# Optimization experiments

Measured on AMD Instinct MI355X. Metric: run time of the kernel, lower is better.

## Reference

```python
import jax, jax.numpy as jnp
import numpy as np

RF = 3          # receptive_field_size (cubic)
STRIDE = 1
TEMP = 1.0      # softmax temperature ('soft' sampling, eval mode: no Gumbel noise)
TREE_DEPTH = 4

# Truth table of all 16 binary gates: GATES[g, t] = value of gate g on input
# pattern t = 2*a + b (a = first child, b = second child), t in {0,1,2,3}.
GATES = np.array([[(g >> t) & 1 for t in range(4)] for g in range(16)],
                 dtype=np.float32)  # (16, 4)


def _lut_eval(a, b, w):
    """Differentiable 2-input LUT. a, b: (B,K,P,nodes); w: (nodes,K,16)."""
    probs = jax.nn.softmax(w / TEMP, axis=-1)          # (nodes,K,16)
    lut = probs @ jnp.asarray(GATES)                   # (nodes,K,4) relaxed truth table
    lut = jnp.moveaxis(lut, 0, 1)[:, None]             # (K,1,nodes,4) -> bcast over B,P
    l0, l1, l2, l3 = lut[..., 0], lut[..., 1], lut[..., 2], lut[..., 3]
    na, nb = 1.0 - a, 1.0 - b
    # E[lut(a,b)] under independent Bernoulli inputs
    return l0 * na * nb + l1 * na * b + l2 * a * nb + l3 * a * b


def setup_inputs() -> dict:
    key = jax.random.key(0)
    ks = jax.random.split(key, 8)
    B, C, H, W, D = 4, 3, 32, 32, 32
    K, S = 32, 16  # num_kernels, lut_rank**tree_depth leaves
    x = jax.random.uniform(ks[0], (B, C, H, W, D), dtype=jnp.float32)
    # (lut_rank=2, K, S, 4) coords (h, w, d, c); rf=3 and channels=3 so all in [0,3)
    kernel_coords = jax.random.randint(ks[1], (2, K, S, 4), 0, 3, dtype=jnp.int32)
    w0 = jax.random.normal(ks[2], (16, K, 16), dtype=jnp.float32)
    w1 = jax.random.normal(ks[3], (8, K, 16), dtype=jnp.float32)
    w2 = jax.random.normal(ks[4], (4, K, 16), dtype=jnp.float32)
    w3 = jax.random.normal(ks[5], (2, K, 16), dtype=jnp.float32)
    w4 = jax.random.normal(ks[6], (1, K, 16), dtype=jnp.float32)
    return {"x": x, "kernel_coords": kernel_coords,
            "w0": w0, "w1": w1, "w2": w2, "w3": w3, "w4": w4}


def reference(x, kernel_coords, w0, w1, w2, w3, w4):
    B, C, H, W, D = x.shape
    OH, OW, OD = (H - RF) // STRIDE + 1, (W - RF) // STRIDE + 1, (D - RF) // STRIDE + 1
    kc = kernel_coords
    # linear offset of each leaf coord inside flattened (C,H,W,D) volume
    base = ((kc[..., 3] * H + kc[..., 0]) * W + kc[..., 1]) * D + kc[..., 2]  # (2,K,S)
    oh = jnp.arange(OH) * STRIDE
    ow = jnp.arange(OW) * STRIDE
    od = jnp.arange(OD) * STRIDE
    patch = ((oh[:, None, None] * W + ow[None, :, None]) * D
             + od[None, None, :]).reshape(-1)                                  # (P,)
    lin = base[:, :, None, :] + patch[None, None, :, None]                     # (2,K,P,S)
    g = x.reshape(B, -1)[:, lin]                                               # (B,2,K,P,S)
    out = _lut_eval(g[:, 0], g[:, 1], w0)                                      # (B,K,P,S)
    for w in (w1, w2, w3, w4):  # binary tree reduction over TREE_DEPTH levels
        out = _lut_eval(out[..., 0::2], out[..., 1::2], w)
    return out.reshape(B, out.shape[1], OH, OW, OD)
```

## Files before the change

### kernel.cpp

```cpp
#include <hip/hip_runtime.h>


#define B_  4
#define C_  3
#define H_  32
#define W_  32
#define D_  32
#define K_  32
#define S_  16
#define WS  33
#define TPB 512

typedef float v8f __attribute__((ext_vector_type(8), aligned(4)));

__device__ __forceinline__ v8f lut8(v8f a, v8f b, float l0, float d1, float d2, float d3) {
    const v8f t0 = a * d2 + l0;
    const v8f t1 = a * d3 + d1;
    return b * t1 + t0;
}

__global__ __launch_bounds__(TPB, 4) void logic_conv3d(
    const float* __restrict__ x,
    const int*   __restrict__ kc,
    const float* __restrict__ w0,
    const float* __restrict__ w1,
    const float* __restrict__ w2,
    const float* __restrict__ w3,
    const float* __restrict__ w4,
    float*       __restrict__ out)
{
    __shared__ float4 s_lut[31];
    __shared__ int    s_lb[16];
    __shared__ int    s_gb[16];
    __shared__ __align__(16) float slab[18 * 32 * WS];

    const int bk  = blockIdx.x;
    const int b   = bk >> 5;
    const int k   = bk & 31;
    const int tid = threadIdx.x;
    const int oh0 = blockIdx.y * 4;

    if (tid < 31) {
        const float* wp; int ln;
        if      (tid < 16) { wp = w0; ln = tid;      }
        else if (tid < 24) { wp = w1; ln = tid - 16; }
        else if (tid < 28) { wp = w2; ln = tid - 24; }
        else if (tid < 30) { wp = w3; ln = tid - 28; }
        else               { wp = w4; ln = 0;        }
        const float* wrow = wp + (ln * K_ + k) * 16;
        float lg[16];
        float m = -1e30f;
        #pragma unroll
        for (int g = 0; g < 16; ++g) { lg[g] = wrow[g]; m = fmaxf(m, lg[g]); }
        float z = 0.f;
        #pragma unroll
        for (int g = 0; g < 16; ++g) { lg[g] = __expf(lg[g] - m); z += lg[g]; }
        const float inv = 1.0f / z;
        float l0 = 0.f, l1 = 0.f, l2 = 0.f, l3 = 0.f;
        #pragma unroll
        for (int g = 0; g < 16; ++g) {
            float p = lg[g] * inv;
            if (g & 1) l0 += p;
            if (g & 2) l1 += p;
            if (g & 4) l2 += p;
            if (g & 8) l3 += p;
        }
        s_lut[tid] = make_float4(l0, l1 - l0, l2 - l0, (l3 - l2) - (l1 - l0));
    } else if (tid >= 32 && tid < 64) {
        const int idx  = tid - 32;
        const int tree = idx >> 4;
        const int s    = idx & 15;
        const int off  = ((tree * K_ + k) * S_ + s) * 4;
        const int h = kc[off + 0], w = kc[off + 1], d = kc[off + 2], c = kc[off + 3];
        if (tree == 0)
            s_lb[s] = ((c * 6 + h) * 32 + w) * WS + d;
        else
            s_gb[s] = ((c * H_ + h) * W_ + w) * D_ + d;
    }

    {
        const float* xb = x + (size_t)b * (C_ * H_ * W_ * D_);
        #pragma unroll
        for (int it = 0; it < 9; ++it) {
            const int idx   = it * TPB + tid;
            const int plane = idx >> 8;
            const int f4    = idx & 255;
            const int c     = plane / 6;
            const int dh    = plane - c * 6;
            const int h     = min(oh0 + dh, H_ - 1);
            const int w     = f4 >> 3;
            const int d4    = (f4 & 7) << 2;
            const float4 val = *(const float4*)(xb + ((c * H_ + h) * W_ + w) * D_ + d4);
            *(float4*)&slab[(plane * 32 + w) * WS + d4] = val;
        }
    }
    __syncthreads();

    int sA[16], sB[16];
    #pragma unroll
    for (int i = 0; i < 4; ++i) {
        const int4 qa = *(const int4*)&s_lb[i * 4];
        sA[i * 4 + 0] = __builtin_amdgcn_readfirstlane(qa.x);
        sA[i * 4 + 1] = __builtin_amdgcn_readfirstlane(qa.y);
        sA[i * 4 + 2] = __builtin_amdgcn_readfirstlane(qa.z);
        sA[i * 4 + 3] = __builtin_amdgcn_readfirstlane(qa.w);
        const int4 qb = *(const int4*)&s_gb[i * 4];
        sB[i * 4 + 0] = __builtin_amdgcn_readfirstlane(qb.x);
        sB[i * 4 + 1] = __builtin_amdgcn_readfirstlane(qb.y);
        sB[i * 4 + 2] = __builtin_amdgcn_readfirstlane(qb.z);
        sB[i * 4 + 3] = __builtin_amdgcn_readfirstlane(qb.w);
    }

    const int ohl = tid >> 7;
    const int r   = tid & 127;
    const int ow  = r >> 2;
    const int gq  = r & 3;
    const int od0 = (gq < 3) ? (gq << 3) : 22;
    const int oh  = oh0 + ohl;

    if (ow < 30 && oh < 30) {
        const int vo  = ohl * (32 * WS) + ow * WS + od0;
        const int gvo = ohl * (W_ * D_) + ow * D_ + od0;
        const float* xg = x + (size_t)b * (C_ * H_ * W_ * D_) + oh0 * (W_ * D_);

        v8f v1[8];
        #pragma unroll
        for (int j = 0; j < 8; ++j) {
            const int s0 = 2 * j, s1 = 2 * j + 1;
            const v8f A0 = *(const v8f*)&slab[sA[s0] + vo];
            const v8f B0 = *(const v8f*)(xg + sB[s0] + gvo);
            const float4 L0 = s_lut[s0];
            const v8f t0 = lut8(A0, B0, L0.x, L0.y, L0.z, L0.w);
            const v8f A1 = *(const v8f*)&slab[sA[s1] + vo];
            const v8f B1 = *(const v8f*)(xg + sB[s1] + gvo);
            const float4 L1 = s_lut[s1];
            const v8f t1 = lut8(A1, B1, L1.x, L1.y, L1.z, L1.w);
            const float4 LN = s_lut[16 + j];
            v1[j] = lut8(t0, t1, LN.x, LN.y, LN.z, LN.w);
        }

        #pragma unroll
        for (int j = 0; j < 4; ++j) {
            const float4 L = s_lut[24 + j];
            v1[j] = lut8(v1[2 * j], v1[2 * j + 1], L.x, L.y, L.z, L.w);
        }
        #pragma unroll
        for (int j = 0; j < 2; ++j) {
            const float4 L = s_lut[28 + j];
            v1[j] = lut8(v1[2 * j], v1[2 * j + 1], L.x, L.y, L.z, L.w);
        }
        {
            const float4 L = s_lut[30];
            v1[0] = lut8(v1[0], v1[1], L.x, L.y, L.z, L.w);
        }

        float* outp = out + (size_t)bk * 27000 + oh * 900 + ow * 30 + od0;
        *(v8f*)outp = v1[0];
    }
}

extern "C" void kernel_launch(void* const* d_in, const int* in_sizes, int n_in,
                              void* d_out, int out_size, void* d_ws, size_t ws_size,
                              hipStream_t stream) {
    const float* x  = (const float*)d_in[0];
    const int*   kc = (const int*)d_in[1];
    const float* w0 = (const float*)d_in[2];
    const float* w1 = (const float*)d_in[3];
    const float* w2 = (const float*)d_in[4];
    const float* w3 = (const float*)d_in[5];
    const float* w4 = (const float*)d_in[6];
    float* out = (float*)d_out;

    dim3 grid(B_ * K_, 8);
    logic_conv3d<<<grid, TPB, 0, stream>>>(x, kc, w0, w1, w2, w3, w4, out);
}
```

Baseline: 82.67 us.

## Process two output kernels per block to reuse the staged input slab

Each block now computes two consecutive kernel indices, loading LUT tables and coordinate offsets for both and reusing the same shared-memory input slab. The grid's first dimension is halved accordingly. This amortizes the global-to-LDS slab load and the block setup over twice the output. The cost is less block-level parallelism and a longer per-thread loop.

```diff
diff --git a/kernel.cpp b/kernel.cpp
--- a/kernel.cpp
+++ b/kernel.cpp
@@ -29,24 +29,27 @@
     const float* __restrict__ w4,
     float*       __restrict__ out)
 {
-    __shared__ float4 s_lut[31];
-    __shared__ int    s_lb[16];
-    __shared__ int    s_gb[16];
+    __shared__ float4 s_lut[2][31];
+    __shared__ __align__(16) int s_lb[2][16];
+    __shared__ __align__(16) int s_gb[2][16];
     __shared__ __align__(16) float slab[18 * 32 * WS];
 
-    const int bk  = blockIdx.x;
-    const int b   = bk >> 5;
-    const int k   = bk & 31;
+    const int bx  = blockIdx.x;
+    const int b   = bx >> 4;
+    const int k0  = (bx & 15) << 1;
     const int tid = threadIdx.x;
     const int oh0 = blockIdx.y * 4;
 
-    if (tid < 31) {
+    if (tid < 62) {
+        const int kk   = (tid >= 31) ? 1 : 0;
+        const int node = tid - kk * 31;
+        const int k    = k0 + kk;
         const float* wp; int ln;
-        if      (tid < 16) { wp = w0; ln = tid;      }
-        else if (tid < 24) { wp = w1; ln = tid - 16; }
-        else if (tid < 28) { wp = w2; ln = tid - 24; }
-        else if (tid < 30) { wp = w3; ln = tid - 28; }
-        else               { wp = w4; ln = 0;        }
+        if      (node < 16) { wp = w0; ln = node;      }
+        else if (node < 24) { wp = w1; ln = node - 16; }
+        else if (node < 28) { wp = w2; ln = node - 24; }
+        else if (node < 30) { wp = w3; ln = node - 28; }
+        else                { wp = w4; ln = 0;         }
         const float* wrow = wp + (ln * K_ + k) * 16;
         float lg[16];
         float m = -1e30f;
@@ -65,17 +68,19 @@
             if (g & 4) l2 += p;
             if (g & 8) l3 += p;
         }
-        s_lut[tid] = make_float4(l0, l1 - l0, l2 - l0, (l3 - l2) - (l1 - l0));
-    } else if (tid >= 32 && tid < 64) {
-        const int idx  = tid - 32;
-        const int tree = idx >> 4;
+        s_lut[kk][node] = make_float4(l0, l1 - l0, l2 - l0, (l3 - l2) - (l1 - l0));
+    } else if (tid >= 64 && tid < 128) {
+        const int idx  = tid - 64;
+        const int kk   = idx >> 5;
+        const int tree = (idx >> 4) & 1;
         const int s    = idx & 15;
+        const int k    = k0 + kk;
         const int off  = ((tree * K_ + k) * S_ + s) * 4;
         const int h = kc[off + 0], w = kc[off + 1], d = kc[off + 2], c = kc[off + 3];
         if (tree == 0)
-            s_lb[s] = ((c * 6 + h) * 32 + w) * WS + d;
+            s_lb[kk][s] = ((c * 6 + h) * 32 + w) * WS + d;
         else
-            s_gb[s] = ((c * H_ + h) * W_ + w) * D_ + d;
+            s_gb[kk][s] = ((c * H_ + h) * W_ + w) * D_ + d;
     }
 
     {
@@ -96,21 +101,6 @@
     }
     __syncthreads();
 
-    int sA[16], sB[16];
-    #pragma unroll
-    for (int i = 0; i < 4; ++i) {
-        const int4 qa = *(const int4*)&s_lb[i * 4];
-        sA[i * 4 + 0] = __builtin_amdgcn_readfirstlane(qa.x);
-        sA[i * 4 + 1] = __builtin_amdgcn_readfirstlane(qa.y);
-        sA[i * 4 + 2] = __builtin_amdgcn_readfirstlane(qa.z);
-        sA[i * 4 + 3] = __builtin_amdgcn_readfirstlane(qa.w);
-        const int4 qb = *(const int4*)&s_gb[i * 4];
-        sB[i * 4 + 0] = __builtin_amdgcn_readfirstlane(qb.x);
-        sB[i * 4 + 1] = __builtin_amdgcn_readfirstlane(qb.y);
-        sB[i * 4 + 2] = __builtin_amdgcn_readfirstlane(qb.z);
-        sB[i * 4 + 3] = __builtin_amdgcn_readfirstlane(qb.w);
-    }
-
     const int ohl = tid >> 7;
     const int r   = tid & 127;
     const int ow  = r >> 2;
@@ -123,39 +113,58 @@
         const int gvo = ohl * (W_ * D_) + ow * D_ + od0;
         const float* xg = x + (size_t)b * (C_ * H_ * W_ * D_) + oh0 * (W_ * D_);
 
-        v8f v1[8];
         #pragma unroll
-        for (int j = 0; j < 8; ++j) {
-            const int s0 = 2 * j, s1 = 2 * j + 1;
-            const v8f A0 = *(const v8f*)&slab[sA[s0] + vo];
-            const v8f B0 = *(const v8f*)(xg + sB[s0] + gvo);
-            const float4 L0 = s_lut[s0];
-            const v8f t0 = lut8(A0, B0, L0.x, L0.y, L0.z, L0.w);
-            const v8f A1 = *(const v8f*)&slab[sA[s1] + vo];
-            const v8f B1 = *(const v8f*)(xg + sB[s1] + gvo);
-            const float4 L1 = s_lut[s1];
-            const v8f t1 = lut8(A1, B1, L1.x, L1.y, L1.z, L1.w);
-            const float4 LN = s_lut[16 + j];
-            v1[j] = lut8(t0, t1, LN.x, LN.y, LN.z, LN.w);
+        for (int kk = 0; kk < 2; ++kk) {
+            int sA[16], sB[16];
+            #pragma unroll
+            for (int i = 0; i < 4; ++i) {
+                const int4 qa = *(const int4*)&s_lb[kk][i * 4];
+                sA[i * 4 + 0] = __builtin_amdgcn_readfirstlane(qa.x);
+                sA[i * 4 + 1] = __builtin_amdgcn_readfirstlane(qa.y);
+                sA[i * 4 + 2] = __builtin_amdgcn_readfirstlane(qa.z);
+                sA[i * 4 + 3] = __builtin_amdgcn_readfirstlane(qa.w);
+                const int4 qb = *(const int4*)&s_gb[kk][i * 4];
+                sB[i * 4 + 0] = __builtin_amdgcn_readfirstlane(qb.x);
+                sB[i * 4 + 1] = __builtin_amdgcn_readfirstlane(qb.y);
+                sB[i * 4 + 2] = __builtin_amdgcn_readfirstlane(qb.z);
+                sB[i * 4 + 3] = __builtin_amdgcn_readfirstlane(qb.w);
+            }
+
+            v8f v1[8];
+            #pragma unroll
+            for (int j = 0; j < 8; ++j) {
+                const int s0 = 2 * j, s1 = 2 * j + 1;
+                const v8f A0 = *(const v8f*)&slab[sA[s0] + vo];
+                const v8f B0 = *(const v8f*)(xg + sB[s0] + gvo);
+                const float4 L0 = s_lut[kk][s0];
+                const v8f t0 = lut8(A0, B0, L0.x, L0.y, L0.z, L0.w);
+                const v8f A1 = *(const v8f*)&slab[sA[s1] + vo];
+                const v8f B1 = *(const v8f*)(xg + sB[s1] + gvo);
+                const float4 L1 = s_lut[kk][s1];
+                const v8f t1 = lut8(A1, B1, L1.x, L1.y, L1.z, L1.w);
+                const float4 LN = s_lut[kk][16 + j];
+                v1[j] = lut8(t0, t1, LN.x, LN.y, LN.z, LN.w);
+            }
+
+            #pragma unroll
+            for (int j = 0; j < 4; ++j) {
+                const float4 L = s_lut[kk][24 + j];
+                v1[j] = lut8(v1[2 * j], v1[2 * j + 1], L.x, L.y, L.z, L.w);
+            }
+            #pragma unroll
+            for (int j = 0; j < 2; ++j) {
+                const float4 L = s_lut[kk][28 + j];
+                v1[j] = lut8(v1[2 * j], v1[2 * j + 1], L.x, L.y, L.z, L.w);
+            }
+            {
+                const float4 L = s_lut[kk][30];
+                v1[0] = lut8(v1[0], v1[1], L.x, L.y, L.z, L.w);
+            }
+
+            const int bk = b * K_ + k0 + kk;
+            float* outp = out + (size_t)bk * 27000 + oh * 900 + ow * 30 + od0;
+            *(v8f*)outp = v1[0];
         }
-
-        #pragma unroll
-        for (int j = 0; j < 4; ++j) {
-            const float4 L = s_lut[24 + j];
-            v1[j] = lut8(v1[2 * j], v1[2 * j + 1], L.x, L.y, L.z, L.w);
-        }
-        #pragma unroll
-        for (int j = 0; j < 2; ++j) {
-            const float4 L = s_lut[28 + j];
-            v1[j] = lut8(v1[2 * j], v1[2 * j + 1], L.x, L.y, L.z, L.w);
-        }
-        {
-            const float4 L = s_lut[30];
-            v1[0] = lut8(v1[0], v1[1], L.x, L.y, L.z, L.w);
-        }
-
-        float* outp = out + (size_t)bk * 27000 + oh * 900 + ow * 30 + od0;
-        *(v8f*)outp = v1[0];
     }
 }
 
@@ -171,6 +180,6 @@
     const float* w4 = (const float*)d_in[6];
     float* out = (float*)d_out;
 
-    dim3 grid(B_ * K_, 8);
+    dim3 grid((B_ * K_) / 2, 8);
     logic_conv3d<<<grid, TPB, 0, stream>>>(x, kc, w0, w1, w2, w3, w4, out);
 }
```

Result: no change. 82.24 us (-0.5%).
